# Kernel tuning notes

Hardware: AMD Instinct MI355X
Metric: run time of the kernel (lower is better)

The kernel has to match this reference:

```python
import jax, jax.numpy as jnp
import numpy as np
import math

LAYER_NUMBER = 2          # coeff for query-key layer scaling
HEAD_DIM = 128
NORM_FACTOR = math.sqrt(HEAD_DIM) * LAYER_NUMBER  # apply_query_key_layer_scaling
COEFF = float(LAYER_NUMBER)
MASK_FILL = -10000.0


def setup_inputs() -> dict:
    key = jax.random.key(0)
    k1, k2, k3, k4 = jax.random.split(key, 4)
    sq, b, nh, hn = 2048, 2, 16, HEAD_DIM
    query_layer = jax.random.normal(k1, (sq, b, nh, hn), dtype=jnp.float32)
    key_layer = jax.random.normal(k2, (sq, b, nh, hn), dtype=jnp.float32)
    value_layer = jax.random.normal(k3, (sq, b, nh, hn), dtype=jnp.float32)
    attention_mask = jax.random.bernoulli(k4, 0.1, (b, 1, sq, sq))
    return {
        "query_layer": query_layer,
        "key_layer": key_layer,
        "value_layer": value_layer,
        "attention_mask": attention_mask,
    }


def reference(query_layer, key_layer, value_layer, attention_mask):
    sq, b, nh, hn = query_layer.shape
    # raw scores: QK^T / norm_factor  -> [b, h, sq, sk]
    scores = jnp.einsum("sbhd,tbhd->bhst", query_layer, key_layer) / NORM_FACTOR
    # MatchedScaleMaskSoftmax: scale by coeff (softmax in fp32), mask-fill, softmax
    x = scores * COEFF
    x = jnp.where(attention_mask, MASK_FILL, x)
    probs = jax.nn.softmax(x, axis=-1)
    # zero out rows where every key is masked
    all_k_masked = jnp.all(attention_mask, axis=-1)  # [b, 1, sq]
    probs = probs * (1.0 - all_k_masked.astype(probs.dtype))[..., None]
    # (dropout p=0.0 -> identity)
    # context: probs @ V -> [sq, b, h, hn] -> [sq, b, hidden]
    ctx = jnp.einsum("bhst,tbhd->sbhd", probs, value_layer)
    return ctx.reshape(sq, b, nh * hn)
```

## Files before the change

### kernel.cpp

```cpp
#include <hip/hip_runtime.h>
#include <math.h>

#define SQ   2048
#define DH   128
#define NKT  32
#define SCALEF  0.08838834764831845f
#define SCALE2  0.12751743f
#define NSHIFT2 (-23.083121f)

typedef __attribute__((ext_vector_type(8))) short bf16x8;
typedef __attribute__((ext_vector_type(4))) float f32x4;

__device__ __forceinline__ unsigned short f2b(float f) {
    unsigned int u = __float_as_uint(f);
    u += 0x7FFFu + ((u >> 16) & 1u);
    return (unsigned short)(u >> 16);
}
__device__ __forceinline__ unsigned int cvtpk(float lo, float hi) {
    unsigned int r;
    asm("v_cvt_pk_bf16_f32 %0, %1, %2" : "=v"(r) : "v"(lo), "v"(hi));
    return r;
}
__device__ __forceinline__ float fexp2(float x) {
    float r;
    asm("v_exp_f32 %0, %1" : "=v"(r) : "v"(x));
    return r;
}

typedef __attribute__((address_space(1))) const unsigned int guint;
typedef __attribute__((address_space(3))) unsigned int luint;
__device__ __forceinline__ void load_lds16(const void* g, void* l) {
    __builtin_amdgcn_global_load_lds((guint*)g, (luint*)l, 16, 0, 0);
}


__global__ __launch_bounds__(256)
void prep_all(const float* __restrict__ K, const float* __restrict__ V,
              const int* __restrict__ M,
              unsigned short* __restrict__ Kp, unsigned short* __restrict__ Vp,
              unsigned long long* __restrict__ B)
{
    const int bid = blockIdx.x;
    const int tid = threadIdx.x;
    if (bid < 4096) {
        int id   = bid * 256 + tid;
        int quad = id & 3;
        int key  = (id >> 2) & 63;
        int ks   = (id >> 8) & 3;
        int kt   = (id >> 10) & 31;
        int bh   = id >> 15;
        int qsrc = quad ^ ((key >> 1) & 3);
        const float* src = K + (size_t)(kt * 64 + key) * 4096 + bh * DH + ks * 32 + qsrc * 8;
        float4 f0 = *(const float4*)src;
        float4 f1 = *(const float4*)(src + 4);
        uint4 o;
        o.x = cvtpk(f0.x, f0.y); o.y = cvtpk(f0.z, f0.w);
        o.z = cvtpk(f1.x, f1.y); o.w = cvtpk(f1.z, f1.w);
        *(uint4*)(Kp + (size_t)id * 8) = o;
    } else if (bid < 6144) {
        int b2   = bid - 4096;
        int t    = b2 >> 1;
        int dhi  = b2 & 1;
        int kt   = t & 31, bh = t >> 5;
        int quad = tid & 3;
        int d2   = tid >> 2;
        int s    = (d2 >> 1) & 3;
        int rb   = (quad ^ s) * 8;
        int d    = dhi * 64 + d2;
        unsigned short* ob = Vp + (size_t)t * 8192;
        #pragma unroll
        for (int ks2 = 0; ks2 < 2; ks2++) {
            const float* vb = V + (size_t)(kt * 64 + ks2 * 32 + rb) * 4096 + bh * DH + d;
            float f[8];
            #pragma unroll
            for (int j = 0; j < 8; j++)
                f[j] = vb[(size_t)j * 4096];
            uint4 o;
            o.x = cvtpk(f[0], f[1]); o.y = cvtpk(f[2], f[3]);
            o.z = cvtpk(f[4], f[5]); o.w = cvtpk(f[6], f[7]);
            *(uint4*)(ob + ((size_t)(ks2 * 128 + d) * 4 + quad) * 8) = o;
        }
    } else {
        int b2   = bid - 6144;
        int wid  = b2 * 4 + (tid >> 6);
        int lane = tid & 63;
        const int* src = M + (size_t)wid * SQ + lane;
        unsigned long long* dst = B + (size_t)wid * NKT;
        #pragma unroll
        for (int t = 0; t < NKT; t++) {
            unsigned long long bm = __ballot(src[t * 64] != 0);
            if (lane == 0) dst[t] = bm;
        }
    }
}

#define STAGE(Kl, Vl, ktt) do {                                              \
    const unsigned short* kg_ = KpT + (size_t)(ktt) * 8192;                  \
    const unsigned short* vg_ = VpT + (size_t)(ktt) * 8192;                  \
    _Pragma("unroll") for (int i_ = 0; i_ < 4; i_++) {                       \
        int ch_ = w * 64 + i_ * 256;                                         \
        load_lds16(kg_ + (size_t)(ch_ + lane) * 8, &Kl[ch_ * 8]);            \
    }                                                                        \
    _Pragma("unroll") for (int i_ = 0; i_ < 4; i_++) {                       \
        int ch_ = w * 64 + i_ * 256;                                         \
        load_lds16(vg_ + (size_t)(ch_ + lane) * 8, &Vl[ch_ * 8]);            \
    }                                                                        \
} while (0)

#define LOADMR(mr, ktt) do {                                                 \
    _Pragma("unroll") for (int r_ = 0; r_ < 4; r_++) {                       \
        mr[0][r_] = mb0[r_ * NKT + (ktt)];                                   \
        mr[1][r_] = mb1[r_ * NKT + (ktt)];                                   \
    }                                                                        \
} while (0)

#define COMPUTE(Kl, Vl, mr) do {                                             \
    f32x4 s[2][4];                                                           \
    _Pragma("unroll") for (int blk = 0; blk < 2; blk++)                      \
        _Pragma("unroll") for (int nb = 0; nb < 4; nb++)                     \
            s[blk][nb] = (f32x4){0.f, 0.f, 0.f, 0.f};                        \
    __builtin_amdgcn_s_setprio(1);                                           \
    _Pragma("unroll") for (int nb = 0; nb < 4; nb++) {                       \
        bf16x8 bk[4];                                                        \
        _Pragma("unroll") for (int ks = 0; ks < 4; ks++)                     \
            bk[ks] = *(const bf16x8*)&Kl[ks * 2048 + nb * 512 + c * 32 + swz8]; \
        _Pragma("unroll") for (int blk = 0; blk < 2; blk++)                  \
            _Pragma("unroll") for (int ks = 0; ks < 4; ks++)                 \
                s[blk][nb] = __builtin_amdgcn_mfma_f32_16x16x32_bf16(aq[blk][ks], bk[ks], s[blk][nb], 0, 0, 0); \
    }                                                                        \
    __builtin_amdgcn_s_setprio(0);                                           \
    _Pragma("unroll") for (int blk = 0; blk < 2; blk++) {                    \
        _Pragma("unroll") for (int r = 0; r < 4; r++) {                      \
            unsigned long long bits = mr[blk][r];                            \
            unsigned wlo = (unsigned)(bits >> c);                            \
            unsigned whi = (unsigned)(bits >> 32) >> c;                      \
            _Pragma("unroll") for (int nbp = 0; nbp < 2; nbp++) {            \
                unsigned wb = nbp ? whi : wlo;                               \
                float p0 = fexp2(fmaf(s[blk][2 * nbp][r],     SCALE2, NSHIFT2)); \
                float p1 = fexp2(fmaf(s[blk][2 * nbp + 1][r], SCALE2, NSHIFT2)); \
                if (wb & 1u)       p0 = 0.0f;                                \
                if (wb & 0x10000u) p1 = 0.0f;                                \
                l[blk][r] += p0 + p1;                                        \
                unsigned pk = cvtpk(p0, p1);                                 \
                int base = nbp * 1024 + blk * 512 + quad * 128 + r * 32 + (c & 7); \
                Pw[base + ((0 + (c >> 3)) ^ quad) * 8] = (unsigned short)pk; \
                Pw[base + ((2 + (c >> 3)) ^ quad) * 8] = (unsigned short)(pk >> 16); \
            }                                                                \
        }                                                                    \
    }                                                                        \
    bf16x8 ap[2][2];                                                         \
    _Pragma("unroll") for (int blk = 0; blk < 2; blk++)                      \
        _Pragma("unroll") for (int ks2 = 0; ks2 < 2; ks2++)                  \
            ap[blk][ks2] = *(const bf16x8*)&Pw[ks2 * 1024 + blk * 512 + c * 32 + ((quad ^ (c >> 2)) * 8)]; \
    __builtin_amdgcn_s_setprio(1);                                           \
    _Pragma("unroll") for (int nb = 0; nb < 8; nb++) {                       \
        bf16x8 bv0 = *(const bf16x8*)&Vl[nb * 512 + c * 32 + swz8];          \
        bf16x8 bv1 = *(const bf16x8*)&Vl[4096 + nb * 512 + c * 32 + swz8];   \
        _Pragma("unroll") for (int blk = 0; blk < 2; blk++) {                \
            oa[blk][nb] = __builtin_amdgcn_mfma_f32_16x16x32_bf16(ap[blk][0], bv0, oa[blk][nb], 0, 0, 0); \
            oa[blk][nb] = __builtin_amdgcn_mfma_f32_16x16x32_bf16(ap[blk][1], bv1, oa[blk][nb], 0, 0, 0); \
        }                                                                    \
    }                                                                        \
    __builtin_amdgcn_s_setprio(0);                                           \
} while (0)

#define PIPE_STEP(Kc, Vc, mrC, Kn, Vn, mrN, ktn) do {                        \
    __builtin_amdgcn_s_barrier();                                            \
    STAGE(Kn, Vn, (ktn));                                                    \
    LOADMR(mrN, (ktn));                                                      \
    asm volatile("s_waitcnt vmcnt(24)" ::: "memory");                        \
    __builtin_amdgcn_s_barrier();                                            \
    asm volatile("" ::: "memory");                                           \
    COMPUTE(Kc, Vc, mrC);                                                    \
} while (0)

__global__ __launch_bounds__(256, 2)
void fa2(const float* __restrict__ Q, const unsigned short* __restrict__ Kp,
         const unsigned short* __restrict__ Vp, const unsigned long long* __restrict__ MB,
         float* __restrict__ out)
{
    __shared__ __align__(16) unsigned short K_lds[2][64 * 128];
    __shared__ __align__(16) unsigned short V_lds[2][64 * 128];
    __shared__ __align__(16) unsigned short P_lds[4 * 2048];

    const int tid  = threadIdx.x;
    const int w    = tid >> 6;
    const int lane = tid & 63;
    const int quad = lane >> 4;
    const int c    = lane & 15;
    const int swz8 = (quad ^ ((c >> 1) & 3)) * 8;

    const int bid0 = blockIdx.x;
    const int bid  = ((bid0 & 7) << 6) | (bid0 >> 3);
    const int qt  = bid & 15;
    const int bh  = bid >> 4;
    const int b_i = bh >> 4;
    const int qbase = qt * 128 + w * 32;
    const size_t bh_off = (size_t)bh * DH;

    bf16x8 aq[2][4];
    #pragma unroll
    for (int blk = 0; blk < 2; blk++) {
        const float* qrow = Q + (size_t)(qbase + blk * 16 + c) * 4096 + bh_off;
        #pragma unroll
        for (int ks = 0; ks < 4; ks++) {
            const int d0 = ks * 32 + quad * 8;
            float4 f0 = *(const float4*)(qrow + d0);
            float4 f1 = *(const float4*)(qrow + d0 + 4);
            uint4 u;
            u.x = cvtpk(f0.x, f0.y); u.y = cvtpk(f0.z, f0.w);
            u.z = cvtpk(f1.x, f1.y); u.w = cvtpk(f1.z, f1.w);
            aq[blk][ks] = *(bf16x8*)&u;
        }
    }

    f32x4 oa[2][8];
    #pragma unroll
    for (int blk = 0; blk < 2; blk++)
        #pragma unroll
        for (int nb = 0; nb < 8; nb++) oa[blk][nb] = (f32x4){0.f, 0.f, 0.f, 0.f};
    float l[2][4];
    #pragma unroll
    for (int blk = 0; blk < 2; blk++)
        #pragma unroll
        for (int r = 0; r < 4; r++) l[blk][r] = 0.0f;

    const unsigned short* KpT = Kp + (size_t)bh * (NKT * 8192);
    const unsigned short* VpT = Vp + (size_t)bh * (NKT * 8192);
    const unsigned long long* mb0 = MB + (size_t)(b_i * SQ + qbase + quad * 4) * NKT;
    const unsigned long long* mb1 = mb0 + 16 * NKT;
    unsigned short* Pw = &P_lds[w * 2048];

    unsigned long long mrA[2][4], mrB[2][4];

    STAGE(K_lds[0], V_lds[0], 0);
    LOADMR(mrA, 0);

    for (int kt = 0; kt < NKT; kt += 2) {
        PIPE_STEP(K_lds[0], V_lds[0], mrA, K_lds[1], V_lds[1], mrB, kt + 1);
        PIPE_STEP(K_lds[1], V_lds[1], mrB, K_lds[0], V_lds[0], mrA, (kt + 2) & 31);
    }
    asm volatile("s_waitcnt vmcnt(0)" ::: "memory");

    #pragma unroll
    for (int blk = 0; blk < 2; blk++) {
        #pragma unroll
        for (int r = 0; r < 4; r++) {
            float t = l[blk][r];
            t += __shfl_xor(t, 1, 64);
            t += __shfl_xor(t, 2, 64);
            t += __shfl_xor(t, 4, 64);
            t += __shfl_xor(t, 8, 64);
            float inv = (t > 0.0f) ? (1.0f / t) : 0.0f;
            float* orow = out + (size_t)(qbase + blk * 16 + quad * 4 + r) * 4096 + bh_off;
            #pragma unroll
            for (int nb = 0; nb < 8; nb++)
                orow[nb * 16 + c] = oa[blk][nb][r] * inv;
        }
    }
}

__global__ __launch_bounds__(256)
void fa_fallback(const float* __restrict__ Q, const float* __restrict__ K,
                 const float* __restrict__ V, const int* __restrict__ mask,
                 float* __restrict__ out)
{
    __shared__ unsigned short K_lds[64 * 136];
    __shared__ unsigned short Vt_lds[128 * 72];
    __shared__ unsigned short P_lds[4 * 16 * 72];
    const int tid = threadIdx.x, w = tid >> 6, lane = tid & 63, quad = lane >> 4, c = lane & 15;
    const int gid = blockIdx.x, qtile = gid & 31, bh = gid >> 5, b_i = bh >> 4;
    const int q0 = qtile * 64 + w * 16;
    const size_t bh_off = (size_t)bh * DH;
    bf16x8 aq[4];
    {
        const float* qrow = Q + (size_t)(q0 + c) * 4096 + bh_off;
        #pragma unroll
        for (int ks = 0; ks < 4; ks++) {
            const int d0 = ks * 32 + quad * 8;
            float4 f0 = *(const float4*)(qrow + d0);
            float4 f1 = *(const float4*)(qrow + d0 + 4);
            bf16x8 a;
            a[0] = (short)f2b(f0.x); a[1] = (short)f2b(f0.y); a[2] = (short)f2b(f0.z); a[3] = (short)f2b(f0.w);
            a[4] = (short)f2b(f1.x); a[5] = (short)f2b(f1.y); a[6] = (short)f2b(f1.z); a[7] = (short)f2b(f1.w);
            aq[ks] = a;
        }
    }
    float m_i[4], l_i[4];
    #pragma unroll
    for (int r = 0; r < 4; r++) { m_i[r] = -INFINITY; l_i[r] = 0.0f; }
    f32x4 o_acc[8];
    #pragma unroll
    for (int nb = 0; nb < 8; nb++) o_acc[nb] = (f32x4){0.f, 0.f, 0.f, 0.f};
    const int srow = tid >> 2, scol = (tid & 3) * 4;
    const int* mbase = mask + (size_t)b_i * SQ * SQ;
    for (int kt = 0; kt < SQ; kt += 64) {
        __syncthreads();
        {
            const float* krow = K + (size_t)(kt + srow) * 4096 + bh_off;
            const float* vrow = V + (size_t)(kt + srow) * 4096 + bh_off;
            #pragma unroll
            for (int j = 0; j < 8; j++) {
                const int d0 = scol + j * 16;
                float4 kf = *(const float4*)(krow + d0);
                unsigned lo = (unsigned)f2b(kf.x) | ((unsigned)f2b(kf.y) << 16);
                unsigned hi = (unsigned)f2b(kf.z) | ((unsigned)f2b(kf.w) << 16);
                *(uint2*)&K_lds[srow * 136 + d0] = make_uint2(lo, hi);
                float4 vf = *(const float4*)(vrow + d0);
                Vt_lds[(d0 + 0) * 72 + srow] = f2b(vf.x);
                Vt_lds[(d0 + 1) * 72 + srow] = f2b(vf.y);
                Vt_lds[(d0 + 2) * 72 + srow] = f2b(vf.z);
                Vt_lds[(d0 + 3) * 72 + srow] = f2b(vf.w);
            }
        }
        __syncthreads();
        f32x4 s[4];
        #pragma unroll
        for (int nb = 0; nb < 4; nb++) s[nb] = (f32x4){0.f, 0.f, 0.f, 0.f};
        #pragma unroll
        for (int nb = 0; nb < 4; nb++)
            #pragma unroll
            for (int ks = 0; ks < 4; ks++) {
                bf16x8 bk = *(const bf16x8*)&K_lds[(nb * 16 + c) * 136 + ks * 32 + quad * 8];
                s[nb] = __builtin_amdgcn_mfma_f32_16x16x32_bf16(aq[ks], bk, s[nb], 0, 0, 0);
            }
        float rowmax[4];
        #pragma unroll
        for (int r = 0; r < 4; r++) rowmax[r] = -INFINITY;
        #pragma unroll
        for (int r = 0; r < 4; r++) {
            const int* mp = mbase + (size_t)(q0 + quad * 4 + r) * SQ + kt + c;
            #pragma unroll
            for (int nb = 0; nb < 4; nb++) {
                float v = s[nb][r] * SCALEF;
                if (mp[nb * 16] != 0) v = -10000.0f;
                s[nb][r] = v;
                rowmax[r] = fmaxf(rowmax[r], v);
            }
        }
        #pragma unroll
        for (int r = 0; r < 4; r++)
            #pragma unroll
            for (int off = 1; off < 16; off <<= 1)
                rowmax[r] = fmaxf(rowmax[r], __shfl_xor(rowmax[r], off, 64));
        float alpha[4], rowsum[4];
        #pragma unroll
        for (int r = 0; r < 4; r++) {
            float mn = fmaxf(m_i[r], rowmax[r]);
            alpha[r] = __expf(m_i[r] - mn);
            m_i[r] = mn;
            rowsum[r] = 0.0f;
        }
        #pragma unroll
        for (int r = 0; r < 4; r++)
            #pragma unroll
            for (int nb = 0; nb < 4; nb++) {
                float p = __expf(s[nb][r] - m_i[r]);
                rowsum[r] += p;
                P_lds[(w * 16 + quad * 4 + r) * 72 + nb * 16 + c] = f2b(p);
            }
        #pragma unroll
        for (int r = 0; r < 4; r++) {
            #pragma unroll
            for (int off = 1; off < 16; off <<= 1)
                rowsum[r] += __shfl_xor(rowsum[r], off, 64);
            l_i[r] = l_i[r] * alpha[r] + rowsum[r];
        }
        #pragma unroll
        for (int nb = 0; nb < 8; nb++)
            #pragma unroll
            for (int r = 0; r < 4; r++) o_acc[nb][r] *= alpha[r];
        bf16x8 ap[2];
        #pragma unroll
        for (int ks = 0; ks < 2; ks++)
            ap[ks] = *(const bf16x8*)&P_lds[(w * 16 + c) * 72 + ks * 32 + quad * 8];
        #pragma unroll
        for (int nb = 0; nb < 8; nb++)
            #pragma unroll
            for (int ks = 0; ks < 2; ks++) {
                bf16x8 bv = *(const bf16x8*)&Vt_lds[(nb * 16 + c) * 72 + ks * 32 + quad * 8];
                o_acc[nb] = __builtin_amdgcn_mfma_f32_16x16x32_bf16(ap[ks], bv, o_acc[nb], 0, 0, 0);
            }
    }
    float inv[4];
    #pragma unroll
    for (int r = 0; r < 4; r++) inv[r] = (m_i[r] > -9999.0f) ? (1.0f / l_i[r]) : 0.0f;
    #pragma unroll
    for (int r = 0; r < 4; r++) {
        float* orow = out + (size_t)(q0 + quad * 4 + r) * 4096 + bh_off;
        #pragma unroll
        for (int nb = 0; nb < 8; nb++) orow[nb * 16 + c] = o_acc[nb][r] * inv[r];
    }
}

extern "C" void kernel_launch(void* const* d_in, const int* in_sizes, int n_in,
                              void* d_out, int out_size, void* d_ws, size_t ws_size,
                              hipStream_t stream) {
    const float* Q    = (const float*)d_in[0];
    const float* K    = (const float*)d_in[1];
    const float* V    = (const float*)d_in[2];
    const int*   mask = (const int*)d_in[3];
    float* out = (float*)d_out;

    const size_t KP_BYTES = (size_t)32 * 32 * 8192 * 2;
    const size_t NEED = 2 * KP_BYTES + (size_t)4096 * NKT * 8;
    if (ws_size < NEED) {
        fa_fallback<<<dim3(1024), dim3(256), 0, stream>>>(Q, K, V, mask, out);
        return;
    }
    unsigned short* Kp = (unsigned short*)d_ws;
    unsigned short* Vp = (unsigned short*)((char*)d_ws + KP_BYTES);
    unsigned long long* MB = (unsigned long long*)((char*)d_ws + 2 * KP_BYTES);

    prep_all<<<dim3(7168), dim3(256), 0, stream>>>(K, V, mask, Kp, Vp, MB);
    fa2<<<dim3(512), dim3(256), 0, stream>>>(Q, Kp, Vp, MB, out);
}
```

Baseline: 265.4 us.

## Keep P in registers via transposed QK^T and 32x32 MFMA for PV

Computes S transposed (K as the A operand) so that each lane holds four consecutive keys for one query row. The probabilities can then be packed and exchanged across lanes with a single xor-16 shuffle instead of a round trip through LDS. The PV product switches to 32x32x16 MFMA with a new V addressing scheme, and the mask loads shrink to one word per query row. This drops the P LDS buffer and its stores and loads, at the cost of cross-lane shuffles, a new output scatter pattern, and a normalization step that goes through LDS.

```diff
diff --git a/kernel.cpp b/kernel.cpp
--- a/kernel.cpp
+++ b/kernel.cpp
@@ -10,6 +10,7 @@
 
 typedef __attribute__((ext_vector_type(8))) short bf16x8;
 typedef __attribute__((ext_vector_type(4))) float f32x4;
+typedef __attribute__((ext_vector_type(16))) float f32x16;
 
 __device__ __forceinline__ unsigned short f2b(float f) {
     unsigned int u = __float_as_uint(f);
@@ -94,6 +95,7 @@
     }
 }
 
+
 #define STAGE(Kl, Vl, ktt) do {                                              \
     const unsigned short* kg_ = KpT + (size_t)(ktt) * 8192;                  \
     const unsigned short* vg_ = VpT + (size_t)(ktt) * 8192;                  \
@@ -108,17 +110,15 @@
 } while (0)
 
 #define LOADMR(mr, ktt) do {                                                 \
-    _Pragma("unroll") for (int r_ = 0; r_ < 4; r_++) {                       \
-        mr[0][r_] = mb0[r_ * NKT + (ktt)];                                   \
-        mr[1][r_] = mb1[r_ * NKT + (ktt)];                                   \
-    }                                                                        \
+    mr[0] = mbq0[(ktt)];                                                     \
+    mr[1] = mbq1[(ktt)];                                                     \
 } while (0)
 
 #define COMPUTE(Kl, Vl, mr) do {                                             \
-    f32x4 s[2][4];                                                           \
+    f32x4 sT[2][4];                                                          \
     _Pragma("unroll") for (int blk = 0; blk < 2; blk++)                      \
         _Pragma("unroll") for (int nb = 0; nb < 4; nb++)                     \
-            s[blk][nb] = (f32x4){0.f, 0.f, 0.f, 0.f};                        \
+            sT[blk][nb] = (f32x4){0.f, 0.f, 0.f, 0.f};                       \
     __builtin_amdgcn_s_setprio(1);                                           \
     _Pragma("unroll") for (int nb = 0; nb < 4; nb++) {                       \
         bf16x8 bk[4];                                                        \
@@ -126,41 +126,73 @@
             bk[ks] = *(const bf16x8*)&Kl[ks * 2048 + nb * 512 + c * 32 + swz8]; \
         _Pragma("unroll") for (int blk = 0; blk < 2; blk++)                  \
             _Pragma("unroll") for (int ks = 0; ks < 4; ks++)                 \
-                s[blk][nb] = __builtin_amdgcn_mfma_f32_16x16x32_bf16(aq[blk][ks], bk[ks], s[blk][nb], 0, 0, 0); \
+                sT[blk][nb] = __builtin_amdgcn_mfma_f32_16x16x32_bf16(bk[ks], aq[blk][ks], sT[blk][nb], 0, 0, 0); \
     }                                                                        \
     __builtin_amdgcn_s_setprio(0);                                           \
-    _Pragma("unroll") for (int blk = 0; blk < 2; blk++) {                    \
-        _Pragma("unroll") for (int r = 0; r < 4; r++) {                      \
-            unsigned long long bits = mr[blk][r];                            \
-            unsigned wlo = (unsigned)(bits >> c);                            \
-            unsigned whi = (unsigned)(bits >> 32) >> c;                      \
-            _Pragma("unroll") for (int nbp = 0; nbp < 2; nbp++) {            \
-                unsigned wb = nbp ? whi : wlo;                               \
-                float p0 = fexp2(fmaf(s[blk][2 * nbp][r],     SCALE2, NSHIFT2)); \
-                float p1 = fexp2(fmaf(s[blk][2 * nbp + 1][r], SCALE2, NSHIFT2)); \
-                if (wb & 1u)       p0 = 0.0f;                                \
-                if (wb & 0x10000u) p1 = 0.0f;                                \
-                l[blk][r] += p0 + p1;                                        \
-                unsigned pk = cvtpk(p0, p1);                                 \
-                int base = nbp * 1024 + blk * 512 + quad * 128 + r * 32 + (c & 7); \
-                Pw[base + ((0 + (c >> 3)) ^ quad) * 8] = (unsigned short)pk; \
-                Pw[base + ((2 + (c >> 3)) ^ quad) * 8] = (unsigned short)(pk >> 16); \
-            }                                                                \
+    unsigned pkA[4][2], pkB[4][2];                                           \
+    {                                                                        \
+        unsigned long long bits = mr[0];                                     \
+        unsigned mlo = (unsigned)(bits >> (quad * 4));                       \
+        unsigned mhi = (unsigned)(bits >> (quad * 4 + 32));                  \
+        _Pragma("unroll") for (int nb = 0; nb < 4; nb++) {                   \
+            unsigned wb = ((nb & 2) ? mhi : mlo) >> ((nb & 1) * 16);         \
+            float p0 = fexp2(fmaf(sT[0][nb][0], SCALE2, NSHIFT2));           \
+            float p1 = fexp2(fmaf(sT[0][nb][1], SCALE2, NSHIFT2));           \
+            float p2 = fexp2(fmaf(sT[0][nb][2], SCALE2, NSHIFT2));           \
+            float p3 = fexp2(fmaf(sT[0][nb][3], SCALE2, NSHIFT2));           \
+            if (wb & 1u) p0 = 0.0f;                                          \
+            if (wb & 2u) p1 = 0.0f;                                          \
+            if (wb & 4u) p2 = 0.0f;                                          \
+            if (wb & 8u) p3 = 0.0f;                                          \
+            l[0] += (p0 + p1) + (p2 + p3);                                   \
+            pkA[nb][0] = cvtpk(p0, p1);                                      \
+            pkA[nb][1] = cvtpk(p2, p3);                                      \
         }                                                                    \
     }                                                                        \
-    bf16x8 ap[2][2];                                                         \
-    _Pragma("unroll") for (int blk = 0; blk < 2; blk++)                      \
-        _Pragma("unroll") for (int ks2 = 0; ks2 < 2; ks2++)                  \
-            ap[blk][ks2] = *(const bf16x8*)&Pw[ks2 * 1024 + blk * 512 + c * 32 + ((quad ^ (c >> 2)) * 8)]; \
+    {                                                                        \
+        unsigned long long bits = mr[1];                                     \
+        unsigned mlo = (unsigned)(bits >> (quad * 4));                       \
+        unsigned mhi = (unsigned)(bits >> (quad * 4 + 32));                  \
+        _Pragma("unroll") for (int nb = 0; nb < 4; nb++) {                   \
+            unsigned wb = ((nb & 2) ? mhi : mlo) >> ((nb & 1) * 16);         \
+            float p0 = fexp2(fmaf(sT[1][nb][0], SCALE2, NSHIFT2));           \
+            float p1 = fexp2(fmaf(sT[1][nb][1], SCALE2, NSHIFT2));           \
+            float p2 = fexp2(fmaf(sT[1][nb][2], SCALE2, NSHIFT2));           \
+            float p3 = fexp2(fmaf(sT[1][nb][3], SCALE2, NSHIFT2));           \
+            if (wb & 1u) p0 = 0.0f;                                          \
+            if (wb & 2u) p1 = 0.0f;                                          \
+            if (wb & 4u) p2 = 0.0f;                                          \
+            if (wb & 8u) p3 = 0.0f;                                          \
+            l[1] += (p0 + p1) + (p2 + p3);                                   \
+            pkB[nb][0] = cvtpk(p0, p1);                                      \
+            pkB[nb][1] = cvtpk(p2, p3);                                      \
+        }                                                                    \
+    }                                                                        \
+    \
+    \
+    unsigned xs[4][2], mn[4][2];                                             \
+    _Pragma("unroll") for (int kc = 0; kc < 4; kc++)                         \
+        _Pragma("unroll") for (int rr = 0; rr < 2; rr++) {                   \
+            unsigned prov = qodd ? pkA[kc][rr] : pkB[kc][rr];                \
+            xs[kc][rr] = __shfl_xor(prov, 16, 64);                           \
+            mn[kc][rr] = qodd ? pkB[kc][rr] : pkA[kc][rr];                   \
+        }                                                                    \
+    \
+    bf16x8 pa[4];                                                            \
+    _Pragma("unroll") for (int kc = 0; kc < 4; kc++) {                       \
+        uint4 u;                                                             \
+        u.x = qodd ? xs[kc][0] : mn[kc][0];                                  \
+        u.y = qodd ? xs[kc][1] : mn[kc][1];                                  \
+        u.z = qodd ? mn[kc][0] : xs[kc][0];                                  \
+        u.w = qodd ? mn[kc][1] : xs[kc][1];                                  \
+        pa[kc] = *(bf16x8*)&u;                                               \
+    }                                                                        \
     __builtin_amdgcn_s_setprio(1);                                           \
-    _Pragma("unroll") for (int nb = 0; nb < 8; nb++) {                       \
-        bf16x8 bv0 = *(const bf16x8*)&Vl[nb * 512 + c * 32 + swz8];          \
-        bf16x8 bv1 = *(const bf16x8*)&Vl[4096 + nb * 512 + c * 32 + swz8];   \
-        _Pragma("unroll") for (int blk = 0; blk < 2; blk++) {                \
-            oa[blk][nb] = __builtin_amdgcn_mfma_f32_16x16x32_bf16(ap[blk][0], bv0, oa[blk][nb], 0, 0, 0); \
-            oa[blk][nb] = __builtin_amdgcn_mfma_f32_16x16x32_bf16(ap[blk][1], bv1, oa[blk][nb], 0, 0, 0); \
+    _Pragma("unroll") for (int dblk = 0; dblk < 4; dblk++)                   \
+        _Pragma("unroll") for (int kc = 0; kc < 4; kc++) {                   \
+            bf16x8 bv = *(const bf16x8*)&Vl[vOff[kc] + dblk * 1024];         \
+            oa32[dblk] = __builtin_amdgcn_mfma_f32_32x32x16_bf16(pa[kc], bv, oa32[dblk], 0, 0, 0); \
         }                                                                    \
-    }                                                                        \
     __builtin_amdgcn_s_setprio(0);                                           \
 } while (0)
 
@@ -168,27 +200,36 @@
     __builtin_amdgcn_s_barrier();                                            \
     STAGE(Kn, Vn, (ktn));                                                    \
     LOADMR(mrN, (ktn));                                                      \
-    asm volatile("s_waitcnt vmcnt(24)" ::: "memory");                        \
+    asm volatile("s_waitcnt vmcnt(12)" ::: "memory");                        \
     __builtin_amdgcn_s_barrier();                                            \
     asm volatile("" ::: "memory");                                           \
     COMPUTE(Kc, Vc, mrC);                                                    \
 } while (0)
 
 __global__ __launch_bounds__(256, 2)
-void fa2(const float* __restrict__ Q, const unsigned short* __restrict__ Kp,
+void fa4(const float* __restrict__ Q, const unsigned short* __restrict__ Kp,
          const unsigned short* __restrict__ Vp, const unsigned long long* __restrict__ MB,
          float* __restrict__ out)
 {
     __shared__ __align__(16) unsigned short K_lds[2][64 * 128];
     __shared__ __align__(16) unsigned short V_lds[2][64 * 128];
-    __shared__ __align__(16) unsigned short P_lds[4 * 2048];
+    __shared__ float lds_inv[4][32];
 
     const int tid  = threadIdx.x;
     const int w    = tid >> 6;
     const int lane = tid & 63;
     const int quad = lane >> 4;
     const int c    = lane & 15;
+    const int w31  = lane & 31;
+    const int hib  = lane >> 5;
+    const bool qodd = (quad & 1);
     const int swz8 = (quad ^ ((c >> 1) & 3)) * 8;
+
+    const int qx = (w31 >> 1) & 3;
+    int vOff[4];
+    #pragma unroll
+    for (int kc = 0; kc < 4; kc++)
+        vOff[kc] = (kc >> 1) * 4096 + w31 * 32 + (((kc & 1) * 2 + hib) ^ qx) * 8;
 
     const int bid0 = blockIdx.x;
     const int bid  = ((bid0 & 7) << 6) | (bid0 >> 3);
@@ -214,24 +255,19 @@
         }
     }
 
-    f32x4 oa[2][8];
-    #pragma unroll
-    for (int blk = 0; blk < 2; blk++)
-        #pragma unroll
-        for (int nb = 0; nb < 8; nb++) oa[blk][nb] = (f32x4){0.f, 0.f, 0.f, 0.f};
-    float l[2][4];
-    #pragma unroll
-    for (int blk = 0; blk < 2; blk++)
-        #pragma unroll
-        for (int r = 0; r < 4; r++) l[blk][r] = 0.0f;
+    f32x16 oa32[4];
+    #pragma unroll
+    for (int dblk = 0; dblk < 4; dblk++)
+        #pragma unroll
+        for (int r = 0; r < 16; r++) oa32[dblk][r] = 0.0f;
+    float l[2] = {0.0f, 0.0f};
 
     const unsigned short* KpT = Kp + (size_t)bh * (NKT * 8192);
     const unsigned short* VpT = Vp + (size_t)bh * (NKT * 8192);
-    const unsigned long long* mb0 = MB + (size_t)(b_i * SQ + qbase + quad * 4) * NKT;
-    const unsigned long long* mb1 = mb0 + 16 * NKT;
-    unsigned short* Pw = &P_lds[w * 2048];
-
-    unsigned long long mrA[2][4], mrB[2][4];
+    const unsigned long long* mbq0 = MB + (size_t)(b_i * SQ + qbase + c) * NKT;
+    const unsigned long long* mbq1 = mbq0 + 16 * NKT;
+
+    unsigned long long mrA[2], mrB[2];
 
     STAGE(K_lds[0], V_lds[0], 0);
     LOADMR(mrA, 0);
@@ -242,20 +278,33 @@
     }
     asm volatile("s_waitcnt vmcnt(0)" ::: "memory");
 
+    float linv[2];
     #pragma unroll
     for (int blk = 0; blk < 2; blk++) {
-        #pragma unroll
-        for (int r = 0; r < 4; r++) {
-            float t = l[blk][r];
-            t += __shfl_xor(t, 1, 64);
-            t += __shfl_xor(t, 2, 64);
-            t += __shfl_xor(t, 4, 64);
-            t += __shfl_xor(t, 8, 64);
-            float inv = (t > 0.0f) ? (1.0f / t) : 0.0f;
-            float* orow = out + (size_t)(qbase + blk * 16 + quad * 4 + r) * 4096 + bh_off;
-            #pragma unroll
-            for (int nb = 0; nb < 8; nb++)
-                orow[nb * 16 + c] = oa[blk][nb][r] * inv;
+        float t = l[blk];
+        t += __shfl_xor(t, 16, 64);
+        t += __shfl_xor(t, 32, 64);
+        linv[blk] = (t > 0.0f) ? (1.0f / t) : 0.0f;
+    }
+    if (quad == 0) {
+        lds_inv[w][c] = linv[0];
+        lds_inv[w][c + 16] = linv[1];
+    }
+    asm volatile("s_waitcnt lgkmcnt(0)" ::: "memory");
+
+    float iv[16];
+    #pragma unroll
+    for (int r = 0; r < 16; r += 2) {
+        int qq = (r & 3) + 8 * (r >> 2) + 4 * hib;
+        float2 v2 = *(const float2*)&lds_inv[w][qq];
+        iv[r] = v2.x; iv[r + 1] = v2.y;
+    }
+    #pragma unroll
+    for (int dblk = 0; dblk < 4; dblk++) {
+        #pragma unroll
+        for (int r = 0; r < 16; r++) {
+            int qq = (r & 3) + 8 * (r >> 2) + 4 * hib;
+            out[(size_t)(qbase + qq) * 4096 + bh_off + dblk * 32 + w31] = oa32[dblk][r] * iv[r];
         }
     }
 }
@@ -413,5 +462,5 @@
     unsigned long long* MB = (unsigned long long*)((char*)d_ws + 2 * KP_BYTES);
 
     prep_all<<<dim3(7168), dim3(256), 0, stream>>>(K, V, mask, Kp, Vp, MB);
-    fa2<<<dim3(512), dim3(256), 0, stream>>>(Q, Kp, Vp, MB, out);
-}
+    fa4<<<dim3(512), dim3(256), 0, stream>>>(Q, Kp, Vp, MB, out);
+}
```

Result: faster. 253.8 us (-4.4%).
